# Optimization experiments

Measured on AMD Instinct MI355X. Metric: run time of the kernel, lower is better.

Reference implementation:

```python
import jax, jax.numpy as jnp
import numpy as np

NUM_EMBEDDINGS = 8192
EMBEDDING_DIM = 256


def setup_inputs() -> dict:
    key = jax.random.key(0)
    kx, kw = jax.random.split(key)
    x = jax.random.normal(kx, (16384, EMBEDDING_DIM), dtype=jnp.float32)
    # nn.Embedding weight initialized uniform(-1/K, 1/K)
    bound = 1.0 / NUM_EMBEDDINGS
    weight = jax.random.uniform(kw, (NUM_EMBEDDINGS, EMBEDDING_DIM),
                                dtype=jnp.float32, minval=-bound, maxval=bound)
    return {"x": x, "weight": weight}


def reference(x, weight):
    # flatten to (N, D)
    flat_x = x.reshape(-1, EMBEDDING_DIM)
    distances = (jnp.sum(flat_x * flat_x, axis=1, keepdims=True)
                 + jnp.sum(weight * weight, axis=1)
                 - 2.0 * jnp.matmul(flat_x, weight.T))
    encoding_indices = jnp.argmin(distances, axis=1)  # (N,)
    quantized = weight[encoding_indices].reshape(x.shape)
    return quantized, encoding_indices
```

## Files before the change

kernel.cpp:

```cpp
#include <hip/hip_runtime.h>
#include <hip/hip_bf16.h>

#define NROWS 16384
#define NCODES 8192
#define DIM 256
#define BM 128
#define SPLITS 2
#define CPB (NCODES / SPLITS)
#define CAP 24
#define MARGIND 1.7e-4f

#define WFRAG_BLOCKS 1024
#define SQ_BLOCKS 1536

typedef __attribute__((ext_vector_type(8))) short bf16x8;
typedef __attribute__((ext_vector_type(4))) float f32x4;

__device__ inline unsigned short f2bf(float f) {
    union { __hip_bfloat16 h; unsigned short u; } cv;
    cv.h = __float2bfloat16(f);
    return cv.u;
}
__device__ inline unsigned f2ord(float f) {
    unsigned u = __float_as_uint(f);
    return u ^ ((u >> 31) ? 0xFFFFFFFFu : 0x80000000u);
}
__device__ inline float ord2f(unsigned u) {
    unsigned v = (u & 0x80000000u) ? (u ^ 0x80000000u) : ~u;
    return __uint_as_float(v);
}

__global__ __launch_bounds__(256)
void prep_kernel(const float* __restrict__ x, const float* __restrict__ w,
                 unsigned short* __restrict__ whf,
                 float* __restrict__ xsq, float* __restrict__ wsq,
                 unsigned long long* __restrict__ best64g) {
    if (blockIdx.x < WFRAG_BLOCKS) {
        int tid = blockIdx.x * 256 + threadIdx.x;
        int L = tid & 63;
        int rest = tid >> 6;
        int k32 = rest & 7;
        int c16 = rest >> 3;
        int code = c16 * 16 + (L & 15);
        int k = k32 * 32 + (L >> 4) * 8;
        const float4* p = reinterpret_cast<const float4*>(w + (size_t)code * DIM + k);
        float4 u0 = p[0], u1 = p[1];
        unsigned short tmp[8];
        tmp[0] = f2bf(u0.x); tmp[1] = f2bf(u0.y); tmp[2] = f2bf(u0.z); tmp[3] = f2bf(u0.w);
        tmp[4] = f2bf(u1.x); tmp[5] = f2bf(u1.y); tmp[6] = f2bf(u1.z); tmp[7] = f2bf(u1.w);
        *reinterpret_cast<uint4*>(whf + (size_t)tid * 8) = *reinterpret_cast<uint4*>(tmp);
    } else {
        int blk = blockIdx.x - WFRAG_BLOCKS;
        int row = blk * 16 + (threadIdx.x >> 4);
        int c = threadIdx.x & 15;
        int j = c & 7, h = c >> 3;
        const float* src = (row < NROWS) ? (x + (size_t)row * DIM)
                                         : (w + (size_t)(row - NROWS) * DIM);
        const float* base = src + h * 128 + j;
        float r = 0.0f;
        #pragma unroll
        for (int g = 0; g < 16; ++g) {
            float v = base[g * 8];
            r = __fadd_rn(r, __fmul_rn(v, v));
        }
        float t;
        t = __shfl_xor(r, 1, 64); r = __fadd_rn(r, t);
        t = __shfl_xor(r, 2, 64); r = __fadd_rn(r, t);
        t = __shfl_xor(r, 4, 64); r = __fadd_rn(r, t);
        t = __shfl_xor(r, 8, 64); r = __fadd_rn(r, t);
        if (c == 0) {
            if (row < NROWS) xsq[row] = r;
            else wsq[row - NROWS] = r;
        }
        if (c == 1 && row < NROWS) best64g[row] = 0xFFFFFFFFFFFFFFFFULL;
    }
}

__global__ __launch_bounds__(512, 2)
void vq_main(const float* __restrict__ x, const float* __restrict__ w,
             const unsigned short* __restrict__ whf,
             const float* __restrict__ wsq, const float* __restrict__ xsq,
             unsigned long long* __restrict__ best64g) {
    __shared__ unsigned short afrag[8 * 8 * 64 * 8];
    __shared__ unsigned rowmax[BM];
    __shared__ int cnt[BM];
    __shared__ int cand[BM][CAP];

    const int tid = threadIdx.x;
    const int lane = tid & 63;
    const int wv = tid >> 6;
    const int lm = lane & 15;
    const int lq = lane >> 4;

    const int blk = blockIdx.x;
    const int xcd = blk & 7;
    const int split = xcd & 1;
    const int rowGroup = (xcd >> 1) * 32 + (blk >> 3);
    const int rowBase = rowGroup * BM;
    const int codeBase = split * CPB;

    if (tid < BM) { rowmax[tid] = 0u; cnt[tid] = 0; }

    {
        const int rg = wv;
        const float* xr = x + (size_t)(rowBase + rg * 16 + lm) * DIM + lq * 8;
        #pragma unroll
        for (int k32 = 0; k32 < 8; ++k32) {
            float4 u0 = *reinterpret_cast<const float4*>(xr + k32 * 32);
            float4 u1 = *reinterpret_cast<const float4*>(xr + k32 * 32 + 4);
            unsigned short t8[8];
            t8[0] = f2bf(u0.x); t8[1] = f2bf(u0.y); t8[2] = f2bf(u0.z); t8[3] = f2bf(u0.w);
            t8[4] = f2bf(u1.x); t8[5] = f2bf(u1.y); t8[6] = f2bf(u1.z); t8[7] = f2bf(u1.w);
            *reinterpret_cast<uint4*>(afrag + ((rg * 8 + k32) * 64 + lane) * 8) =
                *reinterpret_cast<uint4*>(t8);
        }
    }
    __syncthreads();

    const unsigned short* afb = afrag + lane * 8;
    const int waveCode16 = (codeBase >> 4) + wv * 32;

    for (int p = 0; p < 8; ++p) {
        const int pbase16 = waveCode16 + p * 4;
        const unsigned short* wpass = whf + (size_t)pbase16 * 4096 + lane * 8;

        f32x4 acc[8][4];
        #pragma unroll
        for (int rg = 0; rg < 8; ++rg)
            #pragma unroll
            for (int cf = 0; cf < 4; ++cf)
                acc[rg][cf] = (f32x4){0.f, 0.f, 0.f, 0.f};

        bf16x8 bb[2][4];
        #pragma unroll
        for (int cf = 0; cf < 4; ++cf)
            bb[0][cf] = *reinterpret_cast<const bf16x8*>(wpass + cf * 4096);

        #pragma unroll
        for (int k32 = 0; k32 < 8; ++k32) {
            const int cur = k32 & 1;
            if (k32 < 7) {
                #pragma unroll
                for (int cf = 0; cf < 4; ++cf)
                    bb[cur ^ 1][cf] = *reinterpret_cast<const bf16x8*>(
                        wpass + cf * 4096 + (k32 + 1) * 512);
            }
            bf16x8 a[8];
            #pragma unroll
            for (int rg = 0; rg < 8; ++rg)
                a[rg] = *reinterpret_cast<const bf16x8*>(afb + (rg * 8 + k32) * 512);
            #pragma unroll
            for (int cf = 0; cf < 4; ++cf)
                #pragma unroll
                for (int rg = 0; rg < 8; ++rg)
                    acc[rg][cf] = __builtin_amdgcn_mfma_f32_16x16x32_bf16(
                        bb[cur][cf], a[rg], acc[rg][cf], 0, 0, 0);
        }

        #pragma unroll
        for (int rg = 0; rg < 8; ++rg) {
            float m = -__builtin_huge_valf();
            #pragma unroll
            for (int cf = 0; cf < 4; ++cf)
                #pragma unroll
                for (int r = 0; r < 4; ++r)
                    m = fmaxf(m, acc[rg][cf][r]);
            float rm = fmaxf(m, __shfl_xor(m, 16, 64));
            rm = fmaxf(rm, __shfl_xor(rm, 32, 64));
            const int row = rg * 16 + lm;
            if (lq == 0) atomicMax(&rowmax[row], f2ord(rm));
            float limit = ord2f(rowmax[row]) - MARGIND;
            if (m >= limit) {
                #pragma unroll
                for (int cf = 0; cf < 4; ++cf)
                    #pragma unroll
                    for (int r = 0; r < 4; ++r) {
                        if (acc[rg][cf][r] >= limit) {
                            int pos = atomicAdd(&cnt[row], 1);
                            if (pos < CAP)
                                cand[row][pos] = (pbase16 + cf) * 16 + lq * 4 + r;
                        }
                    }
            }
        }
    }
    __syncthreads();

    for (int slot = tid; slot < BM * CAP; slot += 512) {
        int row = slot / CAP, pos = slot - (slot / CAP) * CAP;
        int n = cnt[row] < CAP ? cnt[row] : CAP;
        if (pos < n) {
            int c = cand[row][pos];
            const float* xr = x + (size_t)(rowBase + row) * DIM;
            const float* wr = w + (size_t)c * DIM;
            float d = 0.f;
            for (int k = 0; k < DIM; k += 4) {
                float4 a = *reinterpret_cast<const float4*>(xr + k);
                float4 b = *reinterpret_cast<const float4*>(wr + k);
                d = fmaf(a.x, b.x, d);
                d = fmaf(a.y, b.y, d);
                d = fmaf(a.z, b.z, d);
                d = fmaf(a.w, b.w, d);
            }
            float t1 = __fadd_rn(xsq[rowBase + row], wsq[c]);
            float s = __fsub_rn(t1, __fadd_rn(d, d));
            unsigned long long key =
                ((unsigned long long)__float_as_uint(s) << 32) | (unsigned)c;
            atomicMin(best64g + rowBase + row, key);
        }
    }
}

__global__ __launch_bounds__(256)
void out_kernel(const float* __restrict__ w,
                const unsigned long long* __restrict__ best64g,
                float* __restrict__ out_q, float* __restrict__ out_idx) {
    int r = blockIdx.x * 4 + (threadIdx.x >> 6);
    int lane = threadIdx.x & 63;
    unsigned long long key = best64g[r];
    int idx = (int)(key & 0xFFFFFFFFu);
    float4 v = reinterpret_cast<const float4*>(w + (size_t)idx * DIM)[lane];
    reinterpret_cast<float4*>(out_q + (size_t)r * DIM)[lane] = v;
    if (lane == 0) out_idx[r] = (float)idx;
}

extern "C" void kernel_launch(void* const* d_in, const int* in_sizes, int n_in,
                              void* d_out, int out_size, void* d_ws, size_t ws_size,
                              hipStream_t stream) {
    const float* x = (const float*)d_in[0];
    const float* w = (const float*)d_in[1];
    float* out_q = (float*)d_out;
    float* out_idx = (float*)d_out + (size_t)NROWS * DIM;

    unsigned short* whf = (unsigned short*)d_ws;
    float* wsq = (float*)((char*)d_ws + (size_t)NCODES * DIM * 2);
    float* xsq = wsq + NCODES;
    unsigned long long* best64g = (unsigned long long*)(xsq + NROWS);

    prep_kernel<<<WFRAG_BLOCKS + SQ_BLOCKS, 256, 0, stream>>>(x, w, whf, xsq, wsq, best64g);
    vq_main<<<(NROWS / BM) * SPLITS, 512, 0, stream>>>(x, w, whf, wsq, xsq, best64g);
    out_kernel<<<NROWS / 4, 256, 0, stream>>>(w, best64g, out_q, out_idx);
}
```

Measured before the change: 226.3 us.

## Split codebook four ways with 2x4 wave tiling and overflow fallback

Splits the codebook into four parts per row block instead of two. Waves are rearranged into two row halves by four code quarters, which shrinks the per-wave accumulator tile from 8x4 to 4x2 so launch bounds can request four waves per SIMD for more occupancy. MFMA sections are wrapped in s_setprio, and a new fallback does an exact brute-force search over the split's codes for any row whose candidate list overflows. The trade-off is less A-fragment reuse per wave and more total blocks, which means more partial-result atomics.

```diff
diff --git a/kernel.cpp b/kernel.cpp
--- a/kernel.cpp
+++ b/kernel.cpp
@@ -5,8 +5,9 @@
 #define NCODES 8192
 #define DIM 256
 #define BM 128
-#define SPLITS 2
+#define SPLITS 4
 #define CPB (NCODES / SPLITS)
+#define PASSES 16
 #define CAP 24
 #define MARGIND 1.7e-4f
 
@@ -76,7 +77,7 @@
     }
 }
 
-__global__ __launch_bounds__(512, 2)
+__global__ __launch_bounds__(512, 4)
 void vq_main(const float* __restrict__ x, const float* __restrict__ w,
              const unsigned short* __restrict__ whf,
              const float* __restrict__ wsq, const float* __restrict__ xsq,
@@ -85,21 +86,27 @@
     __shared__ unsigned rowmax[BM];
     __shared__ int cnt[BM];
     __shared__ int cand[BM][CAP];
+    __shared__ int ovf_list[BM];
+    __shared__ int ovf_n;
 
     const int tid = threadIdx.x;
     const int lane = tid & 63;
     const int wv = tid >> 6;
     const int lm = lane & 15;
     const int lq = lane >> 4;
+    const int rowHalf = wv >> 2;
+    const int cq = wv & 3;
 
     const int blk = blockIdx.x;
     const int xcd = blk & 7;
-    const int split = xcd & 1;
-    const int rowGroup = (xcd >> 1) * 32 + (blk >> 3);
+    const int split = xcd & 3;
+    const int rowGroup = (xcd >> 2) * 64 + (blk >> 3);
     const int rowBase = rowGroup * BM;
     const int codeBase = split * CPB;
+    const int codeBase16 = codeBase >> 4;
 
     if (tid < BM) { rowmax[tid] = 0u; cnt[tid] = 0; }
+    if (tid == 0) ovf_n = 0;
 
     {
         const int rg = wv;
@@ -117,23 +124,22 @@
     }
     __syncthreads();
 
-    const unsigned short* afb = afrag + lane * 8;
-    const int waveCode16 = (codeBase >> 4) + wv * 32;
-
-    for (int p = 0; p < 8; ++p) {
-        const int pbase16 = waveCode16 + p * 4;
+    const unsigned short* afb = afrag + ((size_t)rowHalf * 2048 + lane) * 8;
+
+    for (int p = 0; p < PASSES; ++p) {
+        const int pbase16 = codeBase16 + p * 8 + cq * 2;
         const unsigned short* wpass = whf + (size_t)pbase16 * 4096 + lane * 8;
 
-        f32x4 acc[8][4];
-        #pragma unroll
-        for (int rg = 0; rg < 8; ++rg)
-            #pragma unroll
-            for (int cf = 0; cf < 4; ++cf)
+        f32x4 acc[4][2];
+        #pragma unroll
+        for (int rg = 0; rg < 4; ++rg)
+            #pragma unroll
+            for (int cf = 0; cf < 2; ++cf)
                 acc[rg][cf] = (f32x4){0.f, 0.f, 0.f, 0.f};
 
-        bf16x8 bb[2][4];
-        #pragma unroll
-        for (int cf = 0; cf < 4; ++cf)
+        bf16x8 bb[2][2];
+        #pragma unroll
+        for (int cf = 0; cf < 2; ++cf)
             bb[0][cf] = *reinterpret_cast<const bf16x8*>(wpass + cf * 4096);
 
         #pragma unroll
@@ -141,38 +147,40 @@
             const int cur = k32 & 1;
             if (k32 < 7) {
                 #pragma unroll
-                for (int cf = 0; cf < 4; ++cf)
+                for (int cf = 0; cf < 2; ++cf)
                     bb[cur ^ 1][cf] = *reinterpret_cast<const bf16x8*>(
                         wpass + cf * 4096 + (k32 + 1) * 512);
             }
-            bf16x8 a[8];
-            #pragma unroll
-            for (int rg = 0; rg < 8; ++rg)
+            bf16x8 a[4];
+            #pragma unroll
+            for (int rg = 0; rg < 4; ++rg)
                 a[rg] = *reinterpret_cast<const bf16x8*>(afb + (rg * 8 + k32) * 512);
-            #pragma unroll
-            for (int cf = 0; cf < 4; ++cf)
-                #pragma unroll
-                for (int rg = 0; rg < 8; ++rg)
+            __builtin_amdgcn_s_setprio(1);
+            #pragma unroll
+            for (int rg = 0; rg < 4; ++rg)
+                #pragma unroll
+                for (int cf = 0; cf < 2; ++cf)
                     acc[rg][cf] = __builtin_amdgcn_mfma_f32_16x16x32_bf16(
                         bb[cur][cf], a[rg], acc[rg][cf], 0, 0, 0);
-        }
-
-        #pragma unroll
-        for (int rg = 0; rg < 8; ++rg) {
+            __builtin_amdgcn_s_setprio(0);
+        }
+
+        #pragma unroll
+        for (int rg = 0; rg < 4; ++rg) {
             float m = -__builtin_huge_valf();
             #pragma unroll
-            for (int cf = 0; cf < 4; ++cf)
+            for (int cf = 0; cf < 2; ++cf)
                 #pragma unroll
                 for (int r = 0; r < 4; ++r)
                     m = fmaxf(m, acc[rg][cf][r]);
             float rm = fmaxf(m, __shfl_xor(m, 16, 64));
             rm = fmaxf(rm, __shfl_xor(rm, 32, 64));
-            const int row = rg * 16 + lm;
+            const int row = (rowHalf * 4 + rg) * 16 + lm;
             if (lq == 0) atomicMax(&rowmax[row], f2ord(rm));
             float limit = ord2f(rowmax[row]) - MARGIND;
             if (m >= limit) {
                 #pragma unroll
-                for (int cf = 0; cf < 4; ++cf)
+                for (int cf = 0; cf < 2; ++cf)
                     #pragma unroll
                     for (int r = 0; r < 4; ++r) {
                         if (acc[rg][cf][r] >= limit) {
@@ -183,6 +191,12 @@
                     }
             }
         }
+    }
+    __syncthreads();
+
+    if (tid < BM && cnt[tid] > CAP) {
+        int i = atomicAdd(&ovf_n, 1);
+        ovf_list[i] = tid;
     }
     __syncthreads();
 
@@ -209,6 +223,37 @@
             atomicMin(best64g + rowBase + row, key);
         }
     }
+
+    for (int i = wv; i < ovf_n; i += 8) {
+        const int row = ovf_list[i];
+        const float* xr = x + (size_t)(rowBase + row) * DIM;
+        const float xq = xsq[rowBase + row];
+        unsigned long long best = 0xFFFFFFFFFFFFFFFFULL;
+        for (int t = lane; t < CPB; t += 64) {
+            int c = codeBase + t;
+            const float* wr = w + (size_t)c * DIM;
+            float d = 0.f;
+            for (int k = 0; k < DIM; k += 4) {
+                float4 a4 = *reinterpret_cast<const float4*>(xr + k);
+                float4 b4 = *reinterpret_cast<const float4*>(wr + k);
+                d = fmaf(a4.x, b4.x, d);
+                d = fmaf(a4.y, b4.y, d);
+                d = fmaf(a4.z, b4.z, d);
+                d = fmaf(a4.w, b4.w, d);
+            }
+            float t1 = __fadd_rn(xq, wsq[c]);
+            float s = __fsub_rn(t1, __fadd_rn(d, d));
+            unsigned long long key =
+                ((unsigned long long)__float_as_uint(s) << 32) | (unsigned)c;
+            best = best < key ? best : key;
+        }
+        #pragma unroll
+        for (int msk = 32; msk >= 1; msk >>= 1) {
+            unsigned long long o = __shfl_xor(best, msk, 64);
+            best = best < o ? best : o;
+        }
+        if (lane == 0) atomicMin(best64g + rowBase + row, best);
+    }
 }
 
 __global__ __launch_bounds__(256)
```

Result: slower. 358.5 us (+58.4%).
